# Kernel tuning notes

Hardware: AMD Instinct MI355X
Metric: run time of the kernel (lower is better)

The kernel has to match this reference:

```python
import jax, jax.numpy as jnp
import numpy as np

EPS = 1e-3  # eps in grad_pursuit_update_step


def _grad_pursuit(signal, dictionary, target_l0):
    """signal: [B, V], dictionary: [F, V] -> dense weights [B, F] (nonneg)."""
    B, V = signal.shape
    F = dictionary.shape[0]
    rows = jnp.arange(B)

    def step(weights, _):
        # residual = signal - weights @ D         [B, V]
        residual = signal - jnp.einsum('bf,fv->bv', weights, dictionary)
        # inner products with every atom          [B, F]
        inner = jnp.einsum('bv,fv->bf', residual, dictionary)
        idx = jnp.argmax(inner, axis=1)           # [B]
        selected = (weights != 0).at[rows, idx].set(True)
        grad = jnp.where(selected, inner, jnp.zeros((), signal.dtype))  # [B, F]
        c = jnp.einsum('bf,fv->bv', grad, dictionary)                   # [B, V]
        c_sq = jnp.sum(c * c, axis=-1)
        step_size = jnp.sum(c * residual, axis=-1) / jnp.maximum(c_sq, EPS)
        weights = jax.nn.relu(weights + step_size[:, None] * grad)
        return weights, None

    w0 = jnp.zeros((B, F), dtype=signal.dtype)
    weights, _ = jax.lax.scan(step, w0, None, length=target_l0)
    return weights


def _decode(indices, weights, dictionary):
    # embedding-bag sum: gather rows then weighted sum over k
    return jnp.einsum('bk,bkv->bv', weights, dictionary[indices])


def setup_inputs() -> dict:
    key = jax.random.key(0)
    k1, k2, k3, k4, k5 = jax.random.split(key, 5)
    B, D, F = 1024, 1024, 8192
    x = jax.random.normal(k1, (B, D), dtype=jnp.float32)
    y = jax.random.normal(k2, (B, D), dtype=jnp.float32)
    xs = jax.random.normal(k3, (F, D), dtype=jnp.float32)
    xs = xs / jnp.linalg.norm(xs, axis=-1, keepdims=True)  # module stores unit-norm atoms
    ys = jax.random.normal(k4, (F, D), dtype=jnp.float32)
    ys = ys / jnp.linalg.norm(jax.random.normal(k3, (F, D)), axis=-1, keepdims=True)
    mean_y = 0.1 * jax.random.normal(k5, (D,), dtype=jnp.float32)
    return {"x": x, "y": y, "xs": xs, "ys": ys, "mean_y": mean_y, "target_l0": 16}


def reference(x, y, xs, ys, mean_y, target_l0):
    # ITDA.forward with subtract_mean=False, skip_connection=False, fvu_loss=True
    dense = _grad_pursuit(x, xs, target_l0)               # [B, F]
    weights, indices = jax.lax.top_k(dense, target_l0)    # [B, k], [B, k]
    x_rec = _decode(indices, weights, xs)                  # [B, V]
    y_rec = _decode(indices, weights, ys)                  # [B, V]
    l2 = jnp.sum((y - y_rec) ** 2, axis=-1)                # [B]
    total_var = jnp.mean(jnp.sum((y - mean_y) ** 2, axis=-1))
    losses = l2 / total_var
    return weights, indices, x_rec, y_rec, losses
```

## Files before the change

### kernel.cpp

```cpp
#include <hip/hip_runtime.h>
#include <cstdint>
#include <cstddef>

#define B_N 1024
#define V_N 1024
#define F_N 8192
#define NSEL 16
#define NITER 16
#define EPSV 1e-3f
#define WINF 0.008f
#define CANDMAX 64
#define CAND2 256
#define NTILE 64

#define BM 64
#define BN 128
#define BK 32
#define NBN (F_N / BN)

typedef __attribute__((ext_vector_type(4))) float f32x4;
typedef __attribute__((ext_vector_type(8))) short bf16x8;
typedef unsigned short u16;

#define GLDS16(g, l) __builtin_amdgcn_global_load_lds((__attribute__((address_space(1))) void*)(g), (__attribute__((address_space(3))) void*)(l), 16, 0, 0)

__device__ __forceinline__ u16 f2bf(float f) {
  unsigned u = __float_as_uint(f);
  return (u16)((u + 0x7FFFu + ((u >> 16) & 1u)) >> 16);
}

__device__ __forceinline__ float block_sum256(float v, float* sbuf) {
#pragma unroll
  for (int o = 32; o > 0; o >>= 1) v += __shfl_down(v, o, 64);
  int lane = threadIdx.x & 63, wid = threadIdx.x >> 6;
  if (lane == 0) sbuf[wid] = v;
  __syncthreads();
  float r = sbuf[0] + sbuf[1] + sbuf[2] + sbuf[3];
  __syncthreads();
  return r;
}

__device__ __forceinline__ float block_max256(float v, float* sbuf) {
#pragma unroll
  for (int o = 32; o > 0; o >>= 1) v = fmaxf(v, __shfl_down(v, o, 64));
  int lane = threadIdx.x & 63, wid = threadIdx.x >> 6;
  if (lane == 0) sbuf[wid] = v;
  __syncthreads();
  float r = fmaxf(fmaxf(sbuf[0], sbuf[1]), fmaxf(sbuf[2], sbuf[3]));
  __syncthreads();
  return r;
}

__device__ __forceinline__ float wave_tree64(float v) {
#pragma unroll
  for (int o = 32; o > 0; o >>= 1) v += __shfl_down(v, o, 64);
  return v;
}

__device__ __forceinline__ float seq_dot(const float* __restrict__ xrow,
                                         const float* __restrict__ sr) {
  float acc = 0.f;
  for (int k = 0; k < V_N; k += 4) {
    float4 xv = *(const float4*)(xrow + k);
    acc = __builtin_fmaf(xv.x, sr[k + 0], acc);
    acc = __builtin_fmaf(xv.y, sr[k + 1], acc);
    acc = __builtin_fmaf(xv.z, sr[k + 2], acc);
    acc = __builtin_fmaf(xv.w, sr[k + 3], acc);
  }
  return acc;
}

__device__ __forceinline__ void wave_g(const float* __restrict__ xr,
                                       const float* __restrict__ sr,
                                       int lane, float* __restrict__ out) {
  float part[4];
#pragma unroll
  for (int vw = 0; vw < 4; vw++) {
    int vt = vw * 64 + lane;
    float4 xvv = *(const float4*)(xr + vt * 4);
    float4 rl4 = *(const float4*)&sr[vt * 4];
    float p = xvv.x * rl4.x + xvv.y * rl4.y + xvv.z * rl4.z + xvv.w * rl4.w;
    part[vw] = wave_tree64(p);
  }
  if (lane == 0) *out = part[0] + part[1] + part[2] + part[3];
}

__global__ __launch_bounds__(256) void rowvar_kernel(const float* __restrict__ y,
                                                     const float* __restrict__ mean_y,
                                                     float* __restrict__ rowvar,
                                                     int* __restrict__ act_cnt) {
  int b = blockIdx.x, t = threadIdx.x;
  __shared__ float sred[4];
  float4 yv = *(const float4*)(y + (size_t)b * V_N + t * 4);
  float4 mv = *(const float4*)(mean_y + t * 4);
  float dx = yv.x - mv.x, dy = yv.y - mv.y, dz = yv.z - mv.z, dw = yv.w - mv.w;
  float p = dx * dx + dy * dy + dz * dz + dw * dw;
  float s = block_sum256(p, sred);
  if (t == 0) { rowvar[b] = s; act_cnt[b] = 0; }
}

__global__ __launch_bounds__(256) void reduce_var_kernel(const float* __restrict__ rowvar,
                                                         float* __restrict__ totvar) {
  __shared__ float sred[4];
  int t = threadIdx.x;
  float p = 0.f;
#pragma unroll
  for (int i = 0; i < 4; i++) p += rowvar[t * 4 + i];
  float s = block_sum256(p, sred);
  if (t == 0) totvar[0] = s / (float)B_N;
}

__global__ __launch_bounds__(256) void xh_kernel(const float* __restrict__ xs,
                                                 u16* __restrict__ Xh) {
  int b = blockIdx.x, t = threadIdx.x;
  float4 v = *(const float4*)(xs + (size_t)b * V_N + t * 4);
  u16* o = Xh + (size_t)b * V_N + t * 4;
  o[0] = f2bf(v.x); o[1] = f2bf(v.y); o[2] = f2bf(v.z); o[3] = f2bf(v.w);
}

__global__ __launch_bounds__(256) void init_kernel(const float* __restrict__ x,
                                                   float* __restrict__ R,
                                                   u16* __restrict__ Rh,
                                                   float* __restrict__ rn2) {
  int b = blockIdx.x, t = threadIdx.x;
  __shared__ float sred[4];
  float4 v = *(const float4*)(x + (size_t)b * V_N + t * 4);
  *(float4*)(R + (size_t)b * V_N + t * 4) = v;
  u16* o = Rh + (size_t)b * V_N + t * 4;
  o[0] = f2bf(v.x); o[1] = f2bf(v.y); o[2] = f2bf(v.z); o[3] = f2bf(v.w);
  float p = v.x * v.x + v.y * v.y + v.z * v.z + v.w * v.w;
  float s = block_sum256(p, sred);
  if (t == 0) rn2[b] = s;
}

__global__ __launch_bounds__(256) void gemm_scan_kernel(const u16* __restrict__ Rh,
                                                        const u16* __restrict__ Xh,
                                                        float* __restrict__ inner,
                                                        float* __restrict__ pval) {
  __shared__ u16 As[128 * 32];
  __shared__ u16 Bs[128 * 32];
  __shared__ float srmax[128][2];
  const int tid = threadIdx.x;
  const int w = tid >> 6, l = tid & 63;
  const int bn = blockIdx.x, bm = blockIdx.y;
  const int wr = w >> 1, wc = w & 1;
  const int lr = l & 15, lg = l >> 4;

  f32x4 acc[4][4];
#pragma unroll
  for (int m = 0; m < 4; m++)
#pragma unroll
    for (int n = 0; n < 4; n++) acc[m][n] = (f32x4){0.f, 0.f, 0.f, 0.f};

  const u16* Ab = Rh + (size_t)bm * 128 * V_N;
  const u16* Bb = Xh + (size_t)bn * 128 * V_N;
  const int srow = w * 16 + (l >> 2);
  const int scol = (l & 3) * 8;

  for (int k0 = 0; k0 < V_N; k0 += 32) {
#pragma unroll
    for (int i = 0; i < 2; i++) {
      GLDS16(Ab + (size_t)(i * 64 + srow) * V_N + k0 + scol, As + i * 2048 + w * 512);
      GLDS16(Bb + (size_t)(i * 64 + srow) * V_N + k0 + scol, Bs + i * 2048 + w * 512);
    }
    __syncthreads();
    bf16x8 af[4], bfr[4];
#pragma unroll
    for (int m = 0; m < 4; m++) af[m] = *(const bf16x8*)&As[(wr * 64 + m * 16 + lr) * 32 + lg * 8];
#pragma unroll
    for (int n = 0; n < 4; n++) bfr[n] = *(const bf16x8*)&Bs[(wc * 64 + n * 16 + lr) * 32 + lg * 8];
#pragma unroll
    for (int m = 0; m < 4; m++)
#pragma unroll
      for (int n = 0; n < 4; n++)
        acc[m][n] = __builtin_amdgcn_mfma_f32_16x16x32_bf16(af[m], bfr[n], acc[m][n], 0, 0, 0);
    __syncthreads();
  }

#pragma unroll
  for (int m = 0; m < 4; m++) {
    int gm = bm * 128 + wr * 64 + m * 16 + lg * 4;
#pragma unroll
    for (int j = 0; j < 4; j++) {
      float pm = acc[m][0][j];
#pragma unroll
      for (int n = 1; n < 4; n++) pm = fmaxf(pm, acc[m][n][j]);
#pragma unroll
      for (int n = 0; n < 4; n++) {
        int gn = bn * 128 + wc * 64 + n * 16 + lr;
        inner[(size_t)(gm + j) * F_N + gn] = acc[m][n][j];
      }
#pragma unroll
      for (int mk = 1; mk < 16; mk <<= 1) pm = fmaxf(pm, __shfl_xor(pm, mk, 64));
      if (lr == 0) srmax[wr * 64 + m * 16 + lg * 4 + j][wc] = pm;
    }
  }
  __syncthreads();
  if (tid < 128) {
    float v = fmaxf(srmax[tid][0], srmax[tid][1]);
    pval[(size_t)(bm * 128 + tid) * NTILE + bn] = v;
  }
}

__global__ __launch_bounds__(256, 4) void scan_update_kernel(const float* __restrict__ x,
                                                             const float* __restrict__ xs,
                                                             const float* __restrict__ inner,
                                                             const float* __restrict__ pval,
                                                             float* __restrict__ rn2,
                                                             int* __restrict__ act_ids,
                                                             float* __restrict__ act_w,
                                                             int* __restrict__ act_cnt,
                                                             float* __restrict__ R,
                                                             u16* __restrict__ Rh) {
  int b = blockIdx.x, t = threadIdx.x;
  const int lane = t & 63, wid = t >> 6;
  __shared__ float sr[V_N];
  __shared__ float spv[NTILE];
  __shared__ int   shot[NTILE];
  __shared__ int   snhot;
  __shared__ float sred[4];
  __shared__ float smax[4];
  __shared__ float scsqp[4], scrp[4];
  __shared__ int   scand[CAND2];
  __shared__ float scval[CAND2];
  __shared__ float sfv[256];
  __shared__ int   sfi[256];
  __shared__ int   scnt_c;
  __shared__ int   sbii;
  __shared__ float sg[NSEL + 2];
  __shared__ float sw[NSEL + 2];
  __shared__ int   sids[NSEL + 2];
  __shared__ int   ssel[NSEL + 2];
  __shared__ int   scnt, scnt0, sjnew;

  float4 rv = *(const float4*)(R + (size_t)b * V_N + t * 4);
  float4 xrow = *(const float4*)(x + (size_t)b * V_N + t * 4);
  *(float4*)&sr[t * 4] = rv;
  if (t < NTILE) spv[t] = pval[(size_t)b * NTILE + t];
  if (t == 0) {
    scnt_c = 0; snhot = 0;
    int c0 = act_cnt[b]; scnt0 = c0;
    for (int j = 0; j < c0; j++) { sids[j] = act_ids[b * NSEL + j]; sw[j] = act_w[b * NSEL + j]; }
  }
  __syncthreads();

  float M = block_max256(spv[t & (NTILE - 1)], smax);
  float win = WINF * sqrtf(rn2[b]);
  float thr = M - win;

  if (t < NTILE && spv[t] >= thr) { int p = atomicAdd(&snhot, 1); shot[p] = t; }
  __syncthreads();
  int nh = snhot;
  const float* irow = inner + (size_t)b * F_N;
  for (int h = 0; h < nh; h += 2) {
    int hh = h + (t >> 7);
    if (hh < nh) {
      int tt = shot[hh];
      float v = irow[tt * 128 + (t & 127)];
      if (v >= thr) { int p = atomicAdd(&scnt_c, 1); if (p < CAND2) scand[p] = tt * 128 + (t & 127); }
    }
  }
  __syncthreads();
  int total = scnt_c;
  int cnt0 = scnt0;

  if (wid >= 1) {
#pragma unroll
    for (int jj = 0; jj < 6; jj++) {
      int j = (wid - 1) + 3 * jj;
      if (j < cnt0 && sw[j] != 0.f)
        wave_g(xs + (size_t)sids[j] * V_N, sr, lane, &sg[j]);
    }
  } else if (total <= CANDMAX) {
    int nc = total;
    if (nc == 1) {
      if (lane == 0) sbii = scand[0];
    } else {
      if (lane < nc) scval[lane] = seq_dot(xs + (size_t)scand[lane] * V_N, sr);
      if (lane == 0) {
        float bv = scval[0]; int bi = scand[0];
        for (int c = 1; c < nc; c++) {
          float v = scval[c]; int id = scand[c];
          if (v > bv || (v == bv && id < bi)) { bv = v; bi = id; }
        }
        sbii = bi;
      }
    }
  }
  __syncthreads();

  if (total > CANDMAX && total <= CAND2) {
    if (t < total) scval[t] = seq_dot(xs + (size_t)scand[t] * V_N, sr);
    __syncthreads();
    if (t == 0) {
      float bv = scval[0]; int bi = scand[0];
      for (int c = 1; c < total; c++) {
        float v = scval[c]; int id = scand[c];
        if (v > bv || (v == bv && id < bi)) { bv = v; bi = id; }
      }
      sbii = bi;
    }
    __syncthreads();
  } else if (total > CAND2) {
    float bv = -1e30f; int bi = 0x7fffffff;
    for (int f = t; f < F_N; f += 256) {
      float acc = seq_dot(xs + (size_t)f * V_N, sr);
      if (acc > bv) { bv = acc; bi = f; }
    }
    sfv[t] = bv; sfi[t] = bi;
    __syncthreads();
    if (t == 0) {
      float bbv = sfv[0]; int bbi = sfi[0];
      for (int c = 1; c < 256; c++) {
        float v = sfv[c]; int id = sfi[c];
        if (v > bbv || (v == bbv && id < bbi)) { bbv = v; bbi = id; }
      }
      sbii = bbi;
    }
    __syncthreads();
  }

  if (t == 0) {
    int bi = sbii;
    int cnt = cnt0;
    int pos = -1;
    for (int j = 0; j < cnt; j++) if (sids[j] == bi) pos = j;
    if (pos < 0) { pos = cnt; sids[cnt] = bi; sw[cnt] = 0.f; cnt++; }
    for (int j = 0; j < cnt; j++) ssel[j] = (sw[j] != 0.f) || (j == pos) ? 1 : 0;
    for (int j = 0; j < cnt; j++) if (!ssel[j]) sg[j] = 0.f;
    sjnew = (sw[pos] == 0.f) ? pos : -1;
    scnt = cnt;
  }
  __syncthreads();
  int cnt = scnt;

  int jnew = sjnew;
  if (jnew >= 0 && wid == 0)
    wave_g(xs + (size_t)sids[jnew] * V_N, sr, lane, &sg[jnew]);
  __syncthreads();

  float4 rl = *(const float4*)&sr[t * 4];
  float4 xv[NSEL + 1];
#pragma unroll
  for (int j = 0; j < NSEL + 1; j++) {
    int jj = j < cnt ? j : 0;
    xv[j] = *(const float4*)(xs + (size_t)sids[jj] * V_N + t * 4);
  }

  float4 cv = {0.f, 0.f, 0.f, 0.f};
#pragma unroll
  for (int j = 0; j < NSEL + 1; j++) {
    if (j < cnt) {
      if (ssel[j]) {
        float g = sg[j];
        cv.x += g * xv[j].x; cv.y += g * xv[j].y; cv.z += g * xv[j].z; cv.w += g * xv[j].w;
      }
    }
  }
  float pcsq = cv.x * cv.x + cv.y * cv.y + cv.z * cv.z + cv.w * cv.w;
  float pcr  = cv.x * rl.x + cv.y * rl.y + cv.z * rl.z + cv.w * rl.w;
  {
    float s1 = wave_tree64(pcsq);
    float s2 = wave_tree64(pcr);
    if (lane == 0) { scsqp[wid] = s1; scrp[wid] = s2; }
  }
  __syncthreads();

  if (t == 0) {
    float csq = scsqp[0] + scsqp[1] + scsqp[2] + scsqp[3];
    float cr  = scrp[0] + scrp[1] + scrp[2] + scrp[3];
    float step = cr / fmaxf(csq, EPSV);
    for (int j = 0; j < cnt; j++)
      if (ssel[j]) sw[j] = fmaxf(sw[j] + step * sg[j], 0.f);
    for (int j = 0; j < cnt; j++) {
      act_ids[b * NSEL + j] = sids[j];
      act_w[b * NSEL + j] = sw[j];
    }
    act_cnt[b] = cnt;
  }
  __syncthreads();

  float4 r = xrow;
#pragma unroll
  for (int j = 0; j < NSEL + 1; j++) {
    if (j < cnt) {
      float wv = sw[j];
      if (wv != 0.f) {
        r.x -= wv * xv[j].x; r.y -= wv * xv[j].y; r.z -= wv * xv[j].z; r.w -= wv * xv[j].w;
      }
    }
  }
  *(float4*)(R + (size_t)b * V_N + t * 4) = r;
  u16* o = Rh + (size_t)b * V_N + t * 4;
  o[0] = f2bf(r.x); o[1] = f2bf(r.y); o[2] = f2bf(r.z); o[3] = f2bf(r.w);
  float p2 = r.x * r.x + r.y * r.y + r.z * r.z + r.w * r.w;
  float s2 = block_sum256(p2, sred);
  if (t == 0) rn2[b] = s2;
}

__global__ __launch_bounds__(256) void residual_kernel(const float* __restrict__ x,
                                                       const float* __restrict__ xs,
                                                       const int* __restrict__ act_ids,
                                                       const float* __restrict__ act_w,
                                                       const int* __restrict__ act_cnt,
                                                       float* __restrict__ R) {
  int b = blockIdx.x, t = threadIdx.x;
  float4 r = *(const float4*)(x + (size_t)b * V_N + t * 4);
  int cnt = act_cnt[b];
  for (int j = 0; j < cnt; j++) {
    float w = act_w[b * NSEL + j];
    if (w != 0.f) {
      const float* xr = xs + (size_t)act_ids[b * NSEL + j] * V_N;
      float4 xv = *(const float4*)(xr + t * 4);
      r.x -= w * xv.x; r.y -= w * xv.y; r.z -= w * xv.z; r.w -= w * xv.w;
    }
  }
  *(float4*)(R + (size_t)b * V_N + t * 4) = r;
}

__global__ __launch_bounds__(256) void gemm_argmax_kernel(const float* __restrict__ R,
                                                          const float* __restrict__ xs,
                                                          float* __restrict__ pval,
                                                          int* __restrict__ pidx) {
  __shared__ float sA[BK * 68];
  __shared__ float sB[BK * 132];
  __shared__ float sMv[64 * 33];
  __shared__ int   sMi[64 * 33];

  int tid = threadIdx.x;
  int bn = blockIdx.x, bm = blockIdx.y;
  float acc[8][4];
#pragma unroll
  for (int i = 0; i < 8; i++)
#pragma unroll
    for (int j = 0; j < 4; j++) acc[i][j] = 0.f;

  int r0 = (tid >> 5) << 3;
  int n0 = (tid & 31) << 2;
  const float* Rbase = R + (size_t)(bm * BM) * V_N;
  const float* Xbase = xs + (size_t)(bn * BN) * V_N;

  for (int k0 = 0; k0 < V_N; k0 += BK) {
    {
      int m = tid >> 2, kf = (tid & 3) * 4;
      float4 v = *(const float4*)(Rbase + (size_t)m * V_N + k0 + kf);
      sA[(kf + 0) * 68 + m] = v.x; sA[(kf + 1) * 68 + m] = v.y;
      sA[(kf + 2) * 68 + m] = v.z; sA[(kf + 3) * 68 + m] = v.w;
      float4 v2 = *(const float4*)(Rbase + (size_t)m * V_N + k0 + kf + 16);
      sA[(kf + 16) * 68 + m] = v2.x; sA[(kf + 17) * 68 + m] = v2.y;
      sA[(kf + 18) * 68 + m] = v2.z; sA[(kf + 19) * 68 + m] = v2.w;
    }
    {
      int nn = tid >> 3, kf = (tid & 7) * 4;
#pragma unroll
      for (int i = 0; i < 4; i++) {
        int n = nn + i * 32;
        float4 v = *(const float4*)(Xbase + (size_t)n * V_N + k0 + kf);
        sB[(kf + 0) * 132 + n] = v.x; sB[(kf + 1) * 132 + n] = v.y;
        sB[(kf + 2) * 132 + n] = v.z; sB[(kf + 3) * 132 + n] = v.w;
      }
    }
    __syncthreads();
#pragma unroll
    for (int k = 0; k < BK; k++) {
      float4 aL = *(float4*)&sA[k * 68 + r0];
      float4 aH = *(float4*)&sA[k * 68 + r0 + 4];
      float4 bv = *(float4*)&sB[k * 132 + n0];
      float a[8] = {aL.x, aL.y, aL.z, aL.w, aH.x, aH.y, aH.z, aH.w};
      float bb[4] = {bv.x, bv.y, bv.z, bv.w};
#pragma unroll
      for (int i = 0; i < 8; i++)
#pragma unroll
        for (int j = 0; j < 4; j++) acc[i][j] += a[i] * bb[j];
    }
    __syncthreads();
  }

#pragma unroll
  for (int i = 0; i < 8; i++) {
    float bvv = acc[i][0]; int bj = 0;
#pragma unroll
    for (int j = 1; j < 4; j++)
      if (acc[i][j] > bvv) { bvv = acc[i][j]; bj = j; }
    sMv[(r0 + i) * 33 + (tid & 31)] = bvv;
    sMi[(r0 + i) * 33 + (tid & 31)] = bn * BN + n0 + bj;
  }
  __syncthreads();
  if (tid < 64) {
    float bvv = sMv[tid * 33]; int bi = sMi[tid * 33];
    for (int c = 1; c < 32; c++) {
      float v = sMv[tid * 33 + c];
      if (v > bvv) { bvv = v; bi = sMi[tid * 33 + c]; }
    }
    pval[(size_t)(bm * BM + tid) * NBN + bn] = bvv;
    pidx[(size_t)(bm * BM + tid) * NBN + bn] = bi;
  }
}

__global__ __launch_bounds__(256) void combine_update_kernel(const float* __restrict__ R,
                                                             const float* __restrict__ xs,
                                                             const float* __restrict__ pval,
                                                             const int* __restrict__ pidx,
                                                             int* __restrict__ act_ids,
                                                             float* __restrict__ act_w,
                                                             int* __restrict__ act_cnt) {
  int b = blockIdx.x, t = threadIdx.x;
  __shared__ float sr[V_N];
  __shared__ float sred[4];
  __shared__ float sg[NSEL + 1];
  __shared__ float sw[NSEL + 1];
  __shared__ int   sids[NSEL + 1];
  __shared__ int   ssel[NSEL + 1];
  __shared__ int   scnt;

  float4 rv = *(const float4*)(R + (size_t)b * V_N + t * 4);
  *(float4*)&sr[t * 4] = rv;

  if (t == 0) {
    const float* pv = pval + (size_t)b * NBN;
    const int* pi = pidx + (size_t)b * NBN;
    float bv = pv[0]; int bi = pi[0];
    for (int c = 1; c < NBN; c++) {
      float v = pv[c];
      if (v > bv) { bv = v; bi = pi[c]; }
    }
    int cnt = act_cnt[b];
    for (int j = 0; j < cnt; j++) { sids[j] = act_ids[b * NSEL + j]; sw[j] = act_w[b * NSEL + j]; }
    int pos = -1;
    for (int j = 0; j < cnt; j++) if (sids[j] == bi) pos = j;
    if (pos < 0) { pos = cnt; sids[cnt] = bi; sw[cnt] = 0.f; cnt++; }
    for (int j = 0; j < cnt; j++) ssel[j] = (sw[j] != 0.f) || (j == pos) ? 1 : 0;
    scnt = cnt;
  }
  __syncthreads();
  int cnt = scnt;

  for (int j = 0; j < cnt; j++) {
    if (!ssel[j]) { if (t == 0) sg[j] = 0.f; continue; }
    const float* xr = xs + (size_t)sids[j] * V_N;
    float4 xv = *(const float4*)(xr + t * 4);
    float4 rl = *(const float4*)&sr[t * 4];
    float p = xv.x * rl.x + xv.y * rl.y + xv.z * rl.z + xv.w * rl.w;
    float s = block_sum256(p, sred);
    if (t == 0) sg[j] = s;
  }
  __syncthreads();

  float4 cv = {0.f, 0.f, 0.f, 0.f};
  for (int j = 0; j < cnt; j++) {
    if (ssel[j]) {
      float g = sg[j];
      const float* xr = xs + (size_t)sids[j] * V_N;
      float4 xv = *(const float4*)(xr + t * 4);
      cv.x += g * xv.x; cv.y += g * xv.y; cv.z += g * xv.z; cv.w += g * xv.w;
    }
  }
  float4 rl = *(const float4*)&sr[t * 4];
  float pcsq = cv.x * cv.x + cv.y * cv.y + cv.z * cv.z + cv.w * cv.w;
  float pcr  = cv.x * rl.x + cv.y * rl.y + cv.z * rl.z + cv.w * rl.w;
  float csq = block_sum256(pcsq, sred);
  float cr  = block_sum256(pcr, sred);

  if (t == 0) {
    float step = cr / fmaxf(csq, EPSV);
    for (int j = 0; j < cnt; j++)
      if (ssel[j]) sw[j] = fmaxf(sw[j] + step * sg[j], 0.f);
    for (int j = 0; j < cnt; j++) {
      act_ids[b * NSEL + j] = sids[j];
      act_w[b * NSEL + j] = sw[j];
    }
    act_cnt[b] = cnt;
  }
}

__global__ __launch_bounds__(256) void topk_kernel(const int* __restrict__ act_ids,
                                                   const float* __restrict__ act_w,
                                                   const int* __restrict__ act_cnt,
                                                   float* __restrict__ out_w,
                                                   float* __restrict__ out_i) {
  int b = blockIdx.x * blockDim.x + threadIdx.x;
  if (b >= B_N) return;
  int cnt = act_cnt[b];
  int ids[NSEL]; float w[NSEL]; int m = 0;
  for (int j = 0; j < cnt; j++) {
    float wv = act_w[b * NSEL + j];
    if (wv > 0.f) { ids[m] = act_ids[b * NSEL + j]; w[m] = wv; m++; }
  }
  for (int i = 1; i < m; i++) {
    float wv = w[i]; int id = ids[i]; int j = i - 1;
    while (j >= 0 && (w[j] < wv || (w[j] == wv && ids[j] > id))) {
      w[j + 1] = w[j]; ids[j + 1] = ids[j]; j--;
    }
    w[j + 1] = wv; ids[j + 1] = id;
  }
  int nf = 0;
  for (int s = m; s < NSEL; s++) {
    for (;;) {
      bool used = false;
      for (int j = 0; j < m; j++) if (ids[j] == nf) used = true;
      if (!used) break;
      nf++;
    }
    ids[s] = nf; w[s] = 0.f; nf++;
  }
  for (int s = 0; s < NSEL; s++) {
    out_w[b * NSEL + s] = w[s];
    out_i[b * NSEL + s] = (float)ids[s];
  }
}

__global__ __launch_bounds__(256) void decode_kernel(const float* __restrict__ y,
                                                     const float* __restrict__ xs,
                                                     const float* __restrict__ ys,
                                                     const float* __restrict__ out_w,
                                                     const float* __restrict__ out_i,
                                                     const float* __restrict__ totvar,
                                                     float* __restrict__ x_rec,
                                                     float* __restrict__ y_rec,
                                                     float* __restrict__ losses) {
  int b = blockIdx.x, t = threadIdx.x;
  __shared__ float swv[NSEL];
  __shared__ int sid[NSEL];
  __shared__ float sred[4];
  if (t < NSEL) { swv[t] = out_w[b * NSEL + t]; sid[t] = (int)out_i[b * NSEL + t]; }
  __syncthreads();
  float4 xr = {0.f, 0.f, 0.f, 0.f}, yr = {0.f, 0.f, 0.f, 0.f};
  for (int s = 0; s < NSEL; s++) {
    float wv = swv[s];
    if (wv != 0.f) {
      const float* xrow = xs + (size_t)sid[s] * V_N;
      const float* yrow = ys + (size_t)sid[s] * V_N;
      float4 a = *(const float4*)(xrow + t * 4);
      float4 c = *(const float4*)(yrow + t * 4);
      xr.x += wv * a.x; xr.y += wv * a.y; xr.z += wv * a.z; xr.w += wv * a.w;
      yr.x += wv * c.x; yr.y += wv * c.y; yr.z += wv * c.z; yr.w += wv * c.w;
    }
  }
  *(float4*)(x_rec + (size_t)b * V_N + t * 4) = xr;
  *(float4*)(y_rec + (size_t)b * V_N + t * 4) = yr;
  float4 yv = *(const float4*)(y + (size_t)b * V_N + t * 4);
  float dx = yv.x - yr.x, dy = yv.y - yr.y, dz = yv.z - yr.z, dw = yv.w - yr.w;
  float p = dx * dx + dy * dy + dz * dz + dw * dw;
  float l2 = block_sum256(p, sred);
  if (t == 0) losses[b] = l2 / totvar[0];
}

extern "C" void kernel_launch(void* const* d_in, const int* in_sizes, int n_in,
                              void* d_out, int out_size, void* d_ws, size_t ws_size,
                              hipStream_t stream) {
  const float* x      = (const float*)d_in[0];
  const float* y      = (const float*)d_in[1];
  const float* xs     = (const float*)d_in[2];
  const float* ys     = (const float*)d_in[3];
  const float* mean_y = (const float*)d_in[4];
  (void)in_sizes; (void)n_in; (void)out_size;

  float* out    = (float*)d_out;
  float* out_w  = out;
  float* out_i  = out + 16384;
  float* out_xr = out + 32768;
  float* out_yr = out + 32768 + 1048576;
  float* out_ls = out + 32768 + 2097152;

  float* ws = (float*)d_ws;

  const size_t FAST_NEED = (size_t)14257153 * 4;

  if (ws_size >= FAST_NEED) {
    float* R     = ws;
    float* inner = ws + 1048576;
    u16*   Rh    = (u16*)(ws + 9437184);
    u16*   Xh    = (u16*)(ws + 9961472);
    float* rn2   = ws + 14155776;
    int*   aid   = (int*)(ws + 14156800);
    float* aw    = ws + 14173184;
    int*   acn   = (int*)(ws + 14189568);
    float* rv    = ws + 14190592;
    float* tv    = ws + 14191616;
    float* pval  = ws + 14191617;

    rowvar_kernel<<<B_N, 256, 0, stream>>>(y, mean_y, rv, acn);
    reduce_var_kernel<<<1, 256, 0, stream>>>(rv, tv);
    xh_kernel<<<F_N, 256, 0, stream>>>(xs, Xh);
    init_kernel<<<B_N, 256, 0, stream>>>(x, R, Rh, rn2);

    for (int it = 0; it < NITER; it++) {
      gemm_scan_kernel<<<dim3(F_N / 128, B_N / 128), 256, 0, stream>>>(Rh, Xh, inner, pval);
      scan_update_kernel<<<B_N, 256, 0, stream>>>(x, xs, inner, pval, rn2, aid, aw, acn, R, Rh);
    }

    topk_kernel<<<(B_N + 255) / 256, 256, 0, stream>>>(aid, aw, acn, out_w, out_i);
    decode_kernel<<<B_N, 256, 0, stream>>>(y, xs, ys, out_w, out_i, tv, out_xr, out_yr, out_ls);
  } else {
    float* R    = ws;
    float* pval = ws + 1048576;
    int*   pidx = (int*)(ws + 1114112);
    int*   aid  = (int*)(ws + 1179648);
    float* aw   = ws + 1196032;
    int*   acn  = (int*)(ws + 1212416);
    float* rv   = ws + 1213440;
    float* tv   = ws + 1214464;

    rowvar_kernel<<<B_N, 256, 0, stream>>>(y, mean_y, rv, acn);
    reduce_var_kernel<<<1, 256, 0, stream>>>(rv, tv);

    for (int it = 0; it < NITER; it++) {
      residual_kernel<<<B_N, 256, 0, stream>>>(x, xs, aid, aw, acn, R);
      gemm_argmax_kernel<<<dim3(NBN, B_N / BM), 256, 0, stream>>>(R, xs, pval, pidx);
      combine_update_kernel<<<B_N, 256, 0, stream>>>(R, xs, pval, pidx, aid, aw, acn);
    }

    topk_kernel<<<(B_N + 255) / 256, 256, 0, stream>>>(aid, aw, acn, out_w, out_i);
    decode_kernel<<<B_N, 256, 0, stream>>>(y, xs, ys, out_w, out_i, tv, out_xr, out_yr, out_ls);
  }
}
```

Before: 1.072 ms.

## Store GEMM inner products as 8-bit quantized gaps below tile max

The GEMM epilogue no longer writes the full fp32 inner-product matrix. It writes one byte per entry, encoding each value's distance below its row's tile maximum, scaled against the candidate window width. The scan kernel compares these bytes to a per-tile limit to build its candidate list, which cuts inner-matrix write and read traffic by a factor of four. The block index is also remapped so that workgroups sharing a panel are grouped together for better cache reuse. Quantization adds floor-rounding error at the window boundary, so candidate sets may differ slightly.

```diff
diff --git a/kernel.cpp b/kernel.cpp
--- a/kernel.cpp
+++ b/kernel.cpp
@@ -21,6 +21,7 @@
 typedef __attribute__((ext_vector_type(4))) float f32x4;
 typedef __attribute__((ext_vector_type(8))) short bf16x8;
 typedef unsigned short u16;
+typedef unsigned char u8;
 
 #define GLDS16(g, l) __builtin_amdgcn_global_load_lds((__attribute__((address_space(1))) void*)(g), (__attribute__((address_space(3))) void*)(l), 16, 0, 0)
 
@@ -135,14 +136,17 @@
 
 __global__ __launch_bounds__(256) void gemm_scan_kernel(const u16* __restrict__ Rh,
                                                         const u16* __restrict__ Xh,
-                                                        float* __restrict__ inner,
+                                                        const float* __restrict__ rn2,
+                                                        u8* __restrict__ inner8,
                                                         float* __restrict__ pval) {
   __shared__ u16 As[128 * 32];
   __shared__ u16 Bs[128 * 32];
   __shared__ float srmax[128][2];
   const int tid = threadIdx.x;
   const int w = tid >> 6, l = tid & 63;
-  const int bn = blockIdx.x, bm = blockIdx.y;
+  const int flat = blockIdx.y * 64 + blockIdx.x;
+  const int wg = (flat & 7) * 64 + (flat >> 3);
+  const int bn = wg & 63, bm = wg >> 6;
   const int wr = w >> 1, wc = w & 1;
   const int lr = l & 15, lg = l >> 4;
 
@@ -179,17 +183,11 @@
 
 #pragma unroll
   for (int m = 0; m < 4; m++) {
-    int gm = bm * 128 + wr * 64 + m * 16 + lg * 4;
 #pragma unroll
     for (int j = 0; j < 4; j++) {
       float pm = acc[m][0][j];
 #pragma unroll
       for (int n = 1; n < 4; n++) pm = fmaxf(pm, acc[m][n][j]);
-#pragma unroll
-      for (int n = 0; n < 4; n++) {
-        int gn = bn * 128 + wc * 64 + n * 16 + lr;
-        inner[(size_t)(gm + j) * F_N + gn] = acc[m][n][j];
-      }
 #pragma unroll
       for (int mk = 1; mk < 16; mk <<= 1) pm = fmaxf(pm, __shfl_xor(pm, mk, 64));
       if (lr == 0) srmax[wr * 64 + m * 16 + lg * 4 + j][wc] = pm;
@@ -200,11 +198,28 @@
     float v = fmaxf(srmax[tid][0], srmax[tid][1]);
     pval[(size_t)(bm * 128 + tid) * NTILE + bn] = v;
   }
+#pragma unroll
+  for (int m = 0; m < 4; m++) {
+#pragma unroll
+    for (int j = 0; j < 4; j++) {
+      int row = wr * 64 + m * 16 + lg * 4 + j;
+      float rmax = fmaxf(srmax[row][0], srmax[row][1]);
+      float qinv = 250.0f / fmaxf(WINF * sqrtf(rn2[bm * 128 + row]), 1e-20f);
+      int gm = bm * 128 + row;
+#pragma unroll
+      for (int n = 0; n < 4; n++) {
+        int gn = bn * 128 + wc * 64 + n * 16 + lr;
+        float df = floorf((rmax - acc[m][n][j]) * qinv);
+        int u = df >= 254.f ? 254 : (int)df;
+        inner8[(size_t)gm * F_N + gn] = (u8)u;
+      }
+    }
+  }
 }
 
 __global__ __launch_bounds__(256, 4) void scan_update_kernel(const float* __restrict__ x,
                                                              const float* __restrict__ xs,
-                                                             const float* __restrict__ inner,
+                                                             const u8* __restrict__ inner8,
                                                              const float* __restrict__ pval,
                                                              float* __restrict__ rn2,
                                                              int* __restrict__ act_ids,
@@ -247,17 +262,19 @@
   float M = block_max256(spv[t & (NTILE - 1)], smax);
   float win = WINF * sqrtf(rn2[b]);
   float thr = M - win;
+  float qinv = 250.0f / fmaxf(win, 1e-20f);
 
   if (t < NTILE && spv[t] >= thr) { int p = atomicAdd(&snhot, 1); shot[p] = t; }
   __syncthreads();
   int nh = snhot;
-  const float* irow = inner + (size_t)b * F_N;
+  const u8* irow8 = inner8 + (size_t)b * F_N;
   for (int h = 0; h < nh; h += 2) {
     int hh = h + (t >> 7);
     if (hh < nh) {
       int tt = shot[hh];
-      float v = irow[tt * 128 + (t & 127)];
-      if (v >= thr) { int p = atomicAdd(&scnt_c, 1); if (p < CAND2) scand[p] = tt * 128 + (t & 127); }
+      int lim = (int)floorf((spv[tt] - thr) * qinv);
+      int u8v = irow8[tt * 128 + (t & 127)];
+      if (u8v <= lim) { int p = atomicAdd(&scnt_c, 1); if (p < CAND2) scand[p] = tt * 128 + (t & 127); }
     }
   }
   __syncthreads();
@@ -667,17 +684,17 @@
   const size_t FAST_NEED = (size_t)14257153 * 4;
 
   if (ws_size >= FAST_NEED) {
-    float* R     = ws;
-    float* inner = ws + 1048576;
-    u16*   Rh    = (u16*)(ws + 9437184);
-    u16*   Xh    = (u16*)(ws + 9961472);
-    float* rn2   = ws + 14155776;
-    int*   aid   = (int*)(ws + 14156800);
-    float* aw    = ws + 14173184;
-    int*   acn   = (int*)(ws + 14189568);
-    float* rv    = ws + 14190592;
-    float* tv    = ws + 14191616;
-    float* pval  = ws + 14191617;
+    float* R      = ws;
+    u8*    inner8 = (u8*)(ws + 1048576);
+    u16*   Rh     = (u16*)(ws + 9437184);
+    u16*   Xh     = (u16*)(ws + 9961472);
+    float* rn2    = ws + 14155776;
+    int*   aid    = (int*)(ws + 14156800);
+    float* aw     = ws + 14173184;
+    int*   acn    = (int*)(ws + 14189568);
+    float* rv     = ws + 14190592;
+    float* tv     = ws + 14191616;
+    float* pval   = ws + 14191617;
 
     rowvar_kernel<<<B_N, 256, 0, stream>>>(y, mean_y, rv, acn);
     reduce_var_kernel<<<1, 256, 0, stream>>>(rv, tv);
@@ -685,8 +702,8 @@
     init_kernel<<<B_N, 256, 0, stream>>>(x, R, Rh, rn2);
 
     for (int it = 0; it < NITER; it++) {
-      gemm_scan_kernel<<<dim3(F_N / 128, B_N / 128), 256, 0, stream>>>(Rh, Xh, inner, pval);
-      scan_update_kernel<<<B_N, 256, 0, stream>>>(x, xs, inner, pval, rn2, aid, aw, acn, R, Rh);
+      gemm_scan_kernel<<<dim3(F_N / 128, B_N / 128), 256, 0, stream>>>(Rh, Xh, rn2, inner8, pval);
+      scan_update_kernel<<<B_N, 256, 0, stream>>>(x, xs, inner8, pval, rn2, aid, aw, acn, R, Rh);
     }
 
     topk_kernel<<<(B_N + 255) / 256, 256, 0, stream>>>(aid, aw, acn, out_w, out_i);
```

New measurement: 1.105 ms. +3.0%, slower.
